# Kernel optimization log

Hardware: AMD Instinct MI355X
Metric: run time of the kernel (lower is better)

Reference implementation:

```python
import math
import jax, jax.numpy as jnp
import numpy as np
from jax import lax

B, S, D = 2, 1024, 768
H, E, DH = 12, 8, 64          # n_head, num_experts, head dim
KA = 1                        # top-k experts per head (attention)
KF = 2                        # top-k experts per token (FFN)
DFF = 2048
EMA_DECAY = 0.99
CAP_FACTOR = 1.25
NEG_INF = -1e9


def setup_inputs() -> dict:
    key = jax.random.key(0)
    ks = jax.random.split(key, 16)
    sc = 0.02
    x = jax.random.normal(ks[0], (B, S, D), jnp.float32)
    causal = jnp.tril(jnp.ones((S, S), jnp.float32))
    mask = jnp.where(causal > 0, 0.0, NEG_INF).astype(jnp.float32)
    return {
        "x": x,
        "mask": mask,
        "W_q": jax.random.normal(ks[1], (D, D), jnp.float32) * sc,
        "W_k": jax.random.normal(ks[2], (D, D), jnp.float32) * sc,
        "W_v": jax.random.normal(ks[3], (H, E, DH, DH), jnp.float32) * sc,
        "W_o": jax.random.normal(ks[4], (H, E, DH, DH), jnp.float32) * sc,
        "W_router": jax.random.normal(ks[5], (D, H * E), jnp.float32) * sc,
        "g1": jnp.ones((D,), jnp.float32),
        "b1": jnp.zeros((D,), jnp.float32),
        "g2": jnp.ones((D,), jnp.float32),
        "b2": jnp.zeros((D,), jnp.float32),
        "gate_ff": jax.random.normal(ks[6], (D, E), jnp.float32) * sc,
        "W1": jax.random.normal(ks[7], (E, D, DFF), jnp.float32) * sc,
        "W2": jax.random.normal(ks[8], (E, DFF, D), jnp.float32) * sc,
    }


def layer_norm(x, g, b, eps=1e-5):
    m = jnp.mean(x, -1, keepdims=True)
    v = jnp.var(x, -1, keepdims=True)
    return (x - m) * lax.rsqrt(v + eps) * g + b


def head_switch_attention(x, mask, W_q, W_k, W_v, W_o, W_router):
    b, s, d = x.shape
    q = (x @ W_q).reshape(b, s, H, DH)
    k = (x @ W_k).reshape(b, s, H, DH)
    scores = jnp.einsum("bshd,bthd->bhst", q, k) / math.sqrt(DH) + mask
    p_attn = jax.nn.softmax(scores, axis=-1)          # (B,H,S,S)
    gate_logits = (x @ W_router).reshape(b, s, H, E)
    topk_scores, topk_idx = lax.top_k(gate_logits, KA)  # (B,S,H,KA)
    probs = jax.nn.softmax(topk_scores, axis=-1)
    x_h = x.reshape(b, s, H, DH)
    # value projections for all experts (small d_h x d_h GEMMs)
    v_all = jnp.einsum("bshd,hedf->bshef", x_h, W_v)
    y = jnp.zeros_like(x_h)
    hard_counts = jnp.zeros((H, E), jnp.float32)
    for slot in range(KA):
        oh = jax.nn.one_hot(topk_idx[..., slot], E, dtype=x.dtype)  # (B,S,H,E)
        v_sel = jnp.einsum("bshef,bshe->bshf", v_all, oh)
        # faithful to original einsum 'bhst,hbsd->hbtd' (sums over s)
        attn_out = jnp.einsum("bhst,bshf->bthf", p_attn, v_sel)
        o_all = jnp.einsum("bthf,hefg->btheg", attn_out, W_o)
        o_sel = jnp.einsum("btheg,bthe->bthg", o_all, oh)
        y = y + o_sel * probs[..., slot][..., None]
        hard_counts = hard_counts + lax.stop_gradient(oh).sum((0, 1))
    y = y.reshape(b, s, d)
    # EMA buffers start at zero -> ema = (1-decay)*hard/denom
    ema = hard_counts / (b * s * KA) * (1.0 - EMA_DECAY)
    p_lb = ema / (ema.sum() + 1e-9)
    aux = (p_lb * p_lb).sum() * E * H
    return y, aux


def moe_ffn(x, gate_ff, W1, W2):
    b, s, d = x.shape
    gate_logits = x @ gate_ff                      # (B,S,E), eval: no noise
    topk_scores, topk_idx = lax.top_k(gate_logits, KF)
    probs = jax.nn.softmax(topk_scores, axis=-1)   # (B,S,KF)
    capacity = math.ceil(CAP_FACTOR * (b * s) / E)
    flat_idx = topk_idx.reshape(-1)                # (B*S*KF,)
    oh_flat = jax.nn.one_hot(flat_idx, E, dtype=jnp.float32)
    tokens_so_far = jnp.cumsum(oh_flat, axis=0)
    keep = jnp.take_along_axis(tokens_so_far <= capacity, flat_idx[:, None], axis=1)[:, 0]
    probs = probs * keep.reshape(b, s, KF).astype(probs.dtype)
    probs = probs / (probs.sum(-1, keepdims=True) + 1e-9)
    oh = jax.nn.one_hot(topk_idx, E, dtype=probs.dtype)   # (B,S,KF,E)
    w = (probs[..., None] * oh).sum(2).reshape(b * s, E)  # combined weight per (token, expert)
    xf = x.reshape(b * s, d)
    yf = jnp.zeros_like(xf)
    for e in range(E):
        # scaling applied BEFORE ReLU, matching original x_sel = x * weight
        xe = xf * w[:, e:e + 1]
        yf = yf + jnp.maximum(xe @ W1[e], 0.0) @ W2[e]
    token_ctr = ((probs > 0)[..., None].astype(jnp.float32) * oh).sum((0, 1, 2))
    imp_ctr = (probs[..., None] * oh).sum((0, 1, 2))
    aux = ((token_ctr / token_ctr.sum()) * (imp_ctr / imp_ctr.sum())).sum() * E
    return yf.reshape(b, s, d), aux


def reference(x, mask, W_q, W_k, W_v, W_o, W_router, g1, b1, g2, b2, gate_ff, W1, W2):
    # pre-norm transformer block: x + Attn(LN(x)); x + MoEFFN(LN(x))
    a, aux1 = head_switch_attention(layer_norm(x, g1, b1), mask, W_q, W_k, W_v, W_o, W_router)
    x1 = x + a  # dropout is identity in eval
    f, aux2 = moe_ffn(layer_norm(x1, g2, b2), gate_ff, W1, W2)
    return x1 + f, aux1 + aux2
```

## Files before the change

kernel.cpp:

```cpp
#include <hip/hip_runtime.h>
#include <hip/hip_bf16.h>
#include <cstdint>

typedef __hip_bfloat16 bf16;
typedef __attribute__((ext_vector_type(8))) __bf16 bfrag;
typedef __attribute__((ext_vector_type(4))) float f32x4;

#define B_    2
#define S_    1024
#define D_    768
#define H_    12
#define E_    8
#define DH_   64
#define DFF_  2048
#define CAP_  320
#define CAPP_ 384
#define NTOK  (B_*S_)
#define NTH   (NTOK*H_)
#define QKLD  1536

__device__ __forceinline__ void stage16(const bf16* g, bf16* ldsLane){
#if __has_builtin(__builtin_amdgcn_global_load_lds)
  __builtin_amdgcn_global_load_lds((const __attribute__((address_space(1))) unsigned int*)g,
                                   (__attribute__((address_space(3))) unsigned int*)ldsLane, 16, 0, 0);
#else
  *(bfrag*)ldsLane = *(const bfrag*)g;
#endif
}

__global__ __launch_bounds__(256)
void transp_cvt(const float* __restrict__ src, bf16* __restrict__ dst,
                int K, int N, long sSrc, long sDst, int dstRowOff)
{
  src += (long)blockIdx.z*sSrc;
  dst += (long)blockIdx.z*sDst;
  __shared__ float t[32][33];
  int n0 = blockIdx.x*32, k0 = blockIdx.y*32;
  int tx = threadIdx.x & 31, ty = threadIdx.x >> 5;
#pragma unroll
  for (int r=0;r<4;r++){
    int kk = k0 + ty + r*8, nn = n0 + tx;
    t[ty+r*8][tx] = (nn < N) ? src[(long)kk*N + nn] : 0.f;
  }
  __syncthreads();
#pragma unroll
  for (int r=0;r<4;r++){
    int nn = n0 + ty + r*8;
    if (nn < N) dst[(long)(dstRowOff + nn)*K + k0 + tx] = __float2bfloat16(t[tx][ty+r*8]);
  }
}

__global__ __launch_bounds__(256)
void transp_f32(const float* __restrict__ src, float* __restrict__ dst, int K, int N)
{
  __shared__ float t[32][33];
  int n0 = blockIdx.x*32, k0 = blockIdx.y*32;
  int tx = threadIdx.x & 31, ty = threadIdx.x >> 5;
#pragma unroll
  for (int r=0;r<4;r++){
    int kk = k0 + ty + r*8, nn = n0 + tx;
    t[ty+r*8][tx] = (nn < N) ? src[(long)kk*N + nn] : 0.f;
  }
  __syncthreads();
#pragma unroll
  for (int r=0;r<4;r++){
    int nn = n0 + ty + r*8;
    if (nn < N) dst[(long)nn*K + k0 + tx] = t[tx][ty+r*8];
  }
}

__global__ __launch_bounds__(256)
void gemm_bn64(const bf16* __restrict__ A, const bf16* __restrict__ Bt, void* __restrict__ C,
               int M, int N, int K, long sA, long sB, long sC, int relu, int outBf)
{
  A  += (long)blockIdx.z*sA;
  Bt += (long)blockIdx.z*sB;
  int m0 = blockIdx.y*128, n0 = blockIdx.x*64;
  __shared__ bf16 As[128*32];
  __shared__ bf16 Bs[64*32];
  int tid = threadIdx.x;
  int w = tid >> 6, lane = tid & 63;
  int quad = lane >> 4, l16 = lane & 15;
  int wm = w*32;
  f32x4 acc[2][4] = {};
  int srow = (lane >> 2);
  int gsw  = ((lane & 3) ^ (srow & 3))*8;
  const bf16* aBase = A + (long)m0*K;
  const bf16* bBase = Bt + (long)n0*K;
  int xr = (l16 & 3);
  for (int k0=0; k0<K; k0+=32){
#pragma unroll
    for (int j=0;j<2;j++){
      int c = w*2 + j;
      int row = c*16 + srow;
      stage16(aBase + (long)row*K + k0 + gsw, As + c*512 + lane*8);
    }
    {
      int row = w*16 + srow;
      stage16(bBase + (long)row*K + k0 + gsw, Bs + w*512 + lane*8);
    }
    __syncthreads();
    bfrag af[2], bfv[4];
#pragma unroll
    for (int t=0;t<2;t++) af[t]  = *(const bfrag*)(As + (wm + t*16 + l16)*32 + ((quad ^ xr)*8));
#pragma unroll
    for (int t=0;t<4;t++) bfv[t] = *(const bfrag*)(Bs + (t*16 + l16)*32 + ((quad ^ xr)*8));
#pragma unroll
    for (int ti=0;ti<2;ti++)
#pragma unroll
      for (int tj=0;tj<4;tj++)
        acc[ti][tj] = __builtin_amdgcn_mfma_f32_16x16x32_bf16(af[ti], bfv[tj], acc[ti][tj], 0, 0, 0);
    __syncthreads();
  }
  long zoff = (long)blockIdx.z*sC;
  if (outBf){
    bf16* Cb = (bf16*)C + zoff;
#pragma unroll
    for (int ti=0;ti<2;ti++)
#pragma unroll
      for (int tj=0;tj<4;tj++)
#pragma unroll
        for (int r=0;r<4;r++){
          int row = m0 + wm + ti*16 + quad*4 + r;
          int col = n0 + tj*16 + l16;
          float v = acc[ti][tj][r];
          if (relu) v = fmaxf(v, 0.f);
          Cb[(long)row*N + col] = __float2bfloat16(v);
        }
  } else {
    float* Cf = (float*)C + zoff;
#pragma unroll
    for (int ti=0;ti<2;ti++)
#pragma unroll
      for (int tj=0;tj<4;tj++)
#pragma unroll
        for (int r=0;r<4;r++){
          int row = m0 + wm + ti*16 + quad*4 + r;
          int col = n0 + tj*16 + l16;
          float v = acc[ti][tj][r];
          if (relu) v = fmaxf(v, 0.f);
          Cf[(long)row*N + col] = v;
        }
  }
}

__global__ __launch_bounds__(256)
void ln_kernel(const float* __restrict__ src, const float* __restrict__ g, const float* __restrict__ bb,
               float* __restrict__ dstF, bf16* __restrict__ dstB,
               const float* __restrict__ gateW, float* __restrict__ glog2)
{
  int row = blockIdx.x, tid = threadIdx.x;
  __shared__ float red[256];
  __shared__ float gsum[4][E_];
  float v[3];
#pragma unroll
  for (int j=0;j<3;j++) v[j] = src[(long)row*D_ + tid + j*256];
  float s = v[0]+v[1]+v[2];
  red[tid]=s; __syncthreads();
  for (int o=128;o>0;o>>=1){ if(tid<o) red[tid]+=red[tid+o]; __syncthreads(); }
  float mean = red[0]*(1.0f/D_);
  __syncthreads();
  float sq = 0.f;
#pragma unroll
  for (int j=0;j<3;j++){ float d=v[j]-mean; sq += d*d; }
  red[tid]=sq; __syncthreads();
  for (int o=128;o>0;o>>=1){ if(tid<o) red[tid]+=red[tid+o]; __syncthreads(); }
  float rstd = rsqrtf(red[0]*(1.0f/D_) + 1e-5f);
  float ov[3];
#pragma unroll
  for (int j=0;j<3;j++){
    int d = tid + j*256;
    float o = (v[j]-mean)*rstd*g[d] + bb[d];
    ov[j] = o;
    dstF[(long)row*D_+d] = o;
    if (dstB) dstB[(long)row*D_+d] = __float2bfloat16(o);
  }
  if (gateW){
    float gp[E_] = {};
#pragma unroll
    for (int j=0;j<3;j++){
      int d = tid + j*256;
      const float* gw = gateW + (long)d*E_;
#pragma unroll
      for (int e=0;e<E_;e++) gp[e] += ov[j]*gw[e];
    }
#pragma unroll
    for (int off=1; off<64; off<<=1)
#pragma unroll
      for (int e=0;e<E_;e++) gp[e] += __shfl_xor(gp[e], off);
    if ((tid & 63) == 0)
#pragma unroll
      for (int e=0;e<E_;e++) gsum[tid>>6][e] = gp[e];
    __syncthreads();
    if (tid < E_)
      glog2[(long)row*E_ + tid] = gsum[0][tid]+gsum[1][tid]+gsum[2][tid]+gsum[3][tid];
  }
}

#define RTOK 4
__global__ __launch_bounds__(768)
void router_argmax(const float* __restrict__ ln1, const float* __restrict__ WrT,
                   int* __restrict__ eidx, int* __restrict__ gHist)
{
  int tok0 = blockIdx.x*RTOK;
  int tid = threadIdx.x;
  int col = tid >> 3, seg = tid & 7;
  __shared__ float xrow[RTOK][D_];
  __shared__ float logits[RTOK][96];
  for (int i=tid; i<RTOK*D_; i+=768){
    int t = i / D_, dpos = i - t*D_;
    xrow[t][dpos] = ln1[(long)(tok0+t)*D_ + dpos];
  }
  __syncthreads();
  const float* wrow = WrT + (long)col*D_;
  float acc[RTOK] = {};
#pragma unroll
  for (int j=0;j<24;j++){
    int dbase = j*32 + seg*4;
    float4 w = *(const float4*)(wrow + dbase);
#pragma unroll
    for (int t=0;t<RTOK;t++){
      float4 xv = *(const float4*)(&xrow[t][dbase]);
      acc[t] += xv.x*w.x + xv.y*w.y + xv.z*w.z + xv.w*w.w;
    }
  }
#pragma unroll
  for (int off=1; off<8; off<<=1)
#pragma unroll
    for (int t=0;t<RTOK;t++) acc[t] += __shfl_xor(acc[t], off);
  if (seg == 0)
#pragma unroll
    for (int t=0;t<RTOK;t++) logits[t][col] = acc[t];
  __syncthreads();
  if (tid < RTOK*H_){
    int t = tid / H_, h = tid % H_;
    const float* p = &logits[t][h*8];
    float best = p[0]; int bi = 0;
#pragma unroll
    for (int e=1;e<8;e++){ float v=p[e]; if (v > best){ best=v; bi=e; } }
    eidx[(tok0+t)*H_ + h] = bi;
    atomicAdd(&gHist[h*E_ + bi], 1);
  }
}

__global__ __launch_bounds__(64)
void vsel_kernel(const float* __restrict__ ln1, const float* __restrict__ Wv,
                 const int* __restrict__ eidx, bf16* __restrict__ vT)
{
  int blk = blockIdx.x;
  int h = blk % H_, tok = blk / H_;
  int b = tok >> 10, s = tok & 1023;
  int f = threadIdx.x;
  __shared__ float xs[DH_];
  xs[f] = ln1[(long)tok*D_ + h*DH_ + f];
  __syncthreads();
  int e = eidx[blk];
  const float* W = Wv + (long)(h*E_+e)*DH_*DH_;
  float acc = 0.f;
#pragma unroll 8
  for (int d=0; d<DH_; d++) acc += xs[d]*W[d*DH_ + f];
  vT[((long)(b*H_+h)*DH_ + f)*S_ + s] = __float2bfloat16(acc);
}

__global__ __launch_bounds__(256)
void attn_stats_mfma(const bf16* __restrict__ qkB, float* __restrict__ gM, float* __restrict__ gL)
{
  int s0 = blockIdx.x*64;
  int h = blockIdx.y, b = blockIdx.z;
  int tid = threadIdx.x;
  int w = tid >> 6, lane = tid & 63;
  int quad = lane >> 4, l16 = lane & 15;
  int x7 = l16 & 7;
  __shared__ bf16 ldsQ[64*64];
  __shared__ bf16 ldsK[64*64];
  const bf16* qbase = qkB + ((long)(b*S_ + s0))*QKLD + h*DH_;
#pragma unroll
  for (int j=0;j<2;j++){
    int c = j*256 + tid;
    int row = c >> 3;
    int gs = ((c & 7) ^ (row & 7))*8;
    stage16(qbase + (long)row*QKLD + gs, ldsQ + c*8);
  }
  float m_run[4] = {-1e30f,-1e30f,-1e30f,-1e30f};
  float l_run[4] = {0.f,0.f,0.f,0.f};
  const bf16* kbase = qkB + ((long)(b*S_))*QKLD + 768 + h*DH_;
  int ttEnd = s0 >> 6;
  for (int tt=0; tt<=ttEnd; tt++){
    __syncthreads();
#pragma unroll
    for (int j=0;j<2;j++){
      int c = j*256 + tid;
      int row = c >> 3;
      int gs = ((c & 7) ^ (row & 7))*8;
      stage16(kbase + (long)(tt*64 + row)*QKLD + gs, ldsK + c*8);
    }
    __syncthreads();
    bfrag af0 = *(const bfrag*)(ldsQ + (w*16 + l16)*64 + ((quad     ^ x7)*8));
    bfrag af1 = *(const bfrag*)(ldsQ + (w*16 + l16)*64 + (((quad+4) ^ x7)*8));
    f32x4 cfr[4];
#pragma unroll
    for (int j=0;j<4;j++){
      bfrag b0 = *(const bfrag*)(ldsK + (j*16 + l16)*64 + ((quad     ^ x7)*8));
      bfrag b1 = *(const bfrag*)(ldsK + (j*16 + l16)*64 + (((quad+4) ^ x7)*8));
      f32x4 z = {};
      z = __builtin_amdgcn_mfma_f32_16x16x32_bf16(af0, b0, z, 0,0,0);
      z = __builtin_amdgcn_mfma_f32_16x16x32_bf16(af1, b1, z, 0,0,0);
      cfr[j] = z;
    }
#pragma unroll
    for (int r=0;r<4;r++){
      int s_g = s0 + w*16 + quad*4 + r;
      float v[4];
#pragma unroll
      for (int j=0;j<4;j++){
        int t_g = tt*64 + j*16 + l16;
        v[j] = (t_g <= s_g) ? cfr[j][r]*0.125f : -1e30f;
      }
      float mt = fmaxf(fmaxf(v[0],v[1]), fmaxf(v[2],v[3]));
#pragma unroll
      for (int mm=1; mm<16; mm<<=1) mt = fmaxf(mt, __shfl_xor(mt, mm));
      float mn = fmaxf(m_run[r], mt);
      float sum = __expf(v[0]-mn)+__expf(v[1]-mn)+__expf(v[2]-mn)+__expf(v[3]-mn);
#pragma unroll
      for (int mm=1; mm<16; mm<<=1) sum += __shfl_xor(sum, mm);
      l_run[r] = l_run[r]*__expf(m_run[r]-mn) + sum;
      m_run[r] = mn;
    }
  }
  if (l16 == 0){
    long base = ((long)(b*H_ + h))*S_ + s0 + w*16 + quad*4;
#pragma unroll
    for (int r=0;r<4;r++){ gM[base+r] = m_run[r]; gL[base+r] = l_run[r]; }
  }
}

__global__ __launch_bounds__(256)
void attn_pv(const bf16* __restrict__ qkB, const bf16* __restrict__ vT,
             const float* __restrict__ gM, const float* __restrict__ gL, float* __restrict__ aoH)
{
  int t0 = blockIdx.x*64;
  int h = blockIdx.y, b = blockIdx.z;
  int bh = b*H_ + h;
  int tid = threadIdx.x;
  int w = tid >> 6, lane = tid & 63;
  int quad = lane >> 4, l16 = lane & 15;
  int x7 = l16 & 7;
  __shared__ bf16 ldsK[64*64];
  __shared__ bf16 ldsQ[64*64];
  __shared__ bf16 ldsV[64*64];
  __shared__ bf16 ldsS[64*72];
  __shared__ float smx[64], sli[64];
  const bf16* kbase = qkB + ((long)(b*S_ + t0))*QKLD + 768 + h*DH_;
#pragma unroll
  for (int j=0;j<2;j++){
    int c = j*256 + tid;
    int row = c >> 3;
    int gs = ((c & 7) ^ (row & 7))*8;
    stage16(kbase + (long)row*QKLD + gs, ldsK + c*8);
  }
  f32x4 accO[4] = {};
  const bf16* qbase = qkB + ((long)(b*S_))*QKLD + h*DH_;
  const bf16* vbase = vT + ((long)bh*DH_)*S_;
  for (int sb = t0>>6; sb < S_/64; sb++){
    __syncthreads();
#pragma unroll
    for (int j=0;j<2;j++){
      int c = j*256 + tid;
      int row = c >> 3;
      int gs = ((c & 7) ^ (row & 7))*8;
      stage16(qbase + (long)(sb*64 + row)*QKLD + gs, ldsQ + c*8);
      stage16(vbase + (long)row*S_ + sb*64 + gs, ldsV + c*8);
    }
    if (tid < 64){
      smx[tid] = gM[(long)bh*S_ + sb*64 + tid];
      sli[tid] = 1.0f / gL[(long)bh*S_ + sb*64 + tid];
    }
    __syncthreads();
    bfrag af0 = *(const bfrag*)(ldsK + (w*16 + l16)*64 + ((quad     ^ x7)*8));
    bfrag af1 = *(const bfrag*)(ldsK + (w*16 + l16)*64 + (((quad+4) ^ x7)*8));
    f32x4 cs[4];
#pragma unroll
    for (int j=0;j<4;j++){
      bfrag b0 = *(const bfrag*)(ldsQ + (j*16 + l16)*64 + ((quad     ^ x7)*8));
      bfrag b1 = *(const bfrag*)(ldsQ + (j*16 + l16)*64 + (((quad+4) ^ x7)*8));
      f32x4 z = {};
      z = __builtin_amdgcn_mfma_f32_16x16x32_bf16(af0, b0, z, 0,0,0);
      z = __builtin_amdgcn_mfma_f32_16x16x32_bf16(af1, b1, z, 0,0,0);
      cs[j] = z;
    }
#pragma unroll
    for (int j=0;j<4;j++)
#pragma unroll
      for (int r=0;r<4;r++){
        int t_loc = w*16 + quad*4 + r;
        int s_loc = j*16 + l16;
        float wgt = ((t0 + t_loc) <= (sb*64 + s_loc))
                  ? __expf(cs[j][r]*0.125f - smx[s_loc])*sli[s_loc] : 0.f;
        ldsS[t_loc*72 + s_loc] = __float2bfloat16(wgt);
      }
    bfrag pa0 = *(const bfrag*)(ldsS + (w*16 + l16)*72 + quad*8);
    bfrag pa1 = *(const bfrag*)(ldsS + (w*16 + l16)*72 + 32 + quad*8);
#pragma unroll
    for (int j=0;j<4;j++){
      bfrag b0 = *(const bfrag*)(ldsV + (j*16 + l16)*64 + ((quad     ^ x7)*8));
      bfrag b1 = *(const bfrag*)(ldsV + (j*16 + l16)*64 + (((quad+4) ^ x7)*8));
      accO[j] = __builtin_amdgcn_mfma_f32_16x16x32_bf16(pa0, b0, accO[j], 0,0,0);
      accO[j] = __builtin_amdgcn_mfma_f32_16x16x32_bf16(pa1, b1, accO[j], 0,0,0);
    }
  }
#pragma unroll
  for (int j=0;j<4;j++)
#pragma unroll
    for (int r=0;r<4;r++){
      int t_loc = w*16 + quad*4 + r;
      int f = j*16 + l16;
      aoH[((long)bh*S_ + t0 + t_loc)*DH_ + f] = accO[j][r];
    }
}

__global__ __launch_bounds__(64)
void oproj_kernel(const float* __restrict__ aoH, const float* __restrict__ Wo,
                  const int* __restrict__ eidx, const float* __restrict__ x,
                  float* __restrict__ x1)
{
  int blk = blockIdx.x;
  int h = blk % H_, tok = blk / H_;
  int b = tok >> 10, s = tok & 1023;
  int g = threadIdx.x;
  __shared__ float xs[DH_];
  xs[g] = aoH[((long)(b*H_+h)*S_ + s)*DH_ + g];
  __syncthreads();
  int e = eidx[blk];
  const float* W = Wo + (long)(h*E_+e)*DH_*DH_;
  float acc = 0.f;
#pragma unroll 8
  for (int f=0; f<DH_; f++) acc += xs[f]*W[f*DH_ + g];
  long idx = (long)tok*D_ + h*DH_ + g;
  x1[idx] = x[idx] + acc;
}

__global__ __launch_bounds__(256)
void route_kernel(const float* __restrict__ glog2, const int* __restrict__ gHist,
                  int* __restrict__ gI0, int* __restrict__ gI1,
                  int* __restrict__ gPos0, int* __restrict__ gPos1,
                  int* __restrict__ listTok, float* __restrict__ listW,
                  int* __restrict__ gCnt, float* __restrict__ auxOut)
{
  __shared__ unsigned char sI0[NTOK], sI1[NTOK];
  __shared__ float sP0[NTOK], sP1[NTOK];
  __shared__ short sPos0[NTOK], sPos1[NTOK];
  __shared__ int   sScan[256*E_];
  __shared__ int   sHist[H_*E_];
  __shared__ float sImp[E_];
  __shared__ int   sCnt[E_];
  int tid = threadIdx.x;
  if (tid < E_) sImp[tid] = 0.f;
  if (tid < H_*E_) sHist[tid] = gHist[tid];
  for (int i=tid; i<NTOK; i+=256){
    const float* p = glog2 + (long)i*E_;
    float b0 = p[0]; int e0 = 0;
#pragma unroll
    for (int e=1;e<E_;e++){ float vv=p[e]; if (vv > b0){ b0=vv; e0=e; } }
    float b1v = -1e30f; int e1 = 0;
#pragma unroll
    for (int e=0;e<E_;e++){ if (e==e0) continue; float vv=p[e]; if (vv > b1v){ b1v=vv; e1=e; } }
    float ex = __expf(b1v - b0);
    float inv = 1.f/(1.f + ex);
    sI0[i] = (unsigned char)e0; sI1[i] = (unsigned char)e1;
    sP0[i] = inv; sP1[i] = ex*inv;
    gI0[i] = e0; gI1[i] = e1;
  }
  __syncthreads();
  {
    int myCnt[E_] = {};
#pragma unroll
    for (int j=0;j<16;j++){
      int i = tid*16 + j;
      int tok = i >> 1;
      int e = (i & 1) ? (int)sI1[tok] : (int)sI0[tok];
      myCnt[e]++;
    }
#pragma unroll
    for (int e=0;e<E_;e++) sScan[tid*E_+e] = myCnt[e];
    __syncthreads();
    for (int off=1; off<256; off<<=1){
      int v[E_];
      if (tid >= off){
#pragma unroll
        for (int e=0;e<E_;e++) v[e] = sScan[(tid-off)*E_+e];
      }
      __syncthreads();
      if (tid >= off){
#pragma unroll
        for (int e=0;e<E_;e++) sScan[tid*E_+e] += v[e];
      }
      __syncthreads();
    }
    int pref[E_];
#pragma unroll
    for (int e=0;e<E_;e++) pref[e] = tid ? sScan[(tid-1)*E_+e] : 0;
#pragma unroll
    for (int j=0;j<16;j++){
      int i = tid*16 + j;
      int tok = i >> 1;
      int e = (i & 1) ? (int)sI1[tok] : (int)sI0[tok];
      int pos = pref[e]++;
      short p = (pos < CAP_) ? (short)pos : (short)-1;
      if (i & 1) sPos1[tok] = p; else sPos0[tok] = p;
    }
    if (tid < E_){
      int cnt = sScan[255*E_ + tid];
      sCnt[tid] = cnt < CAP_ ? cnt : CAP_;
      gCnt[tid] = sCnt[tid];
    }
  }
  __syncthreads();
  for (int i=tid; i<NTOK; i+=256){
    int e0 = sI0[i], e1 = sI1[i];
    int p0i = sPos0[i], p1i = sPos1[i];
    float k0 = p0i >= 0 ? 1.f : 0.f, k1 = p1i >= 0 ? 1.f : 0.f;
    float p0 = sP0[i], p1 = sP1[i];
    float denom = p0*k0 + p1*k1 + 1e-9f;
    float w0 = p0*k0/denom, w1 = p1*k1/denom;
    if (p0i >= 0){ listTok[e0*CAP_+p0i] = i; listW[e0*CAP_+p0i] = w0; atomicAdd(&sImp[e0], w0); }
    if (p1i >= 0){ listTok[e1*CAP_+p1i] = i; listW[e1*CAP_+p1i] = w1; atomicAdd(&sImp[e1], w1); }
    gPos0[i] = p0i; gPos1[i] = p1i;
  }
  __syncthreads();
  if (tid == 0){
    float tot = 0.f;
    for (int i=0;i<H_*E_;i++) tot += (float)sHist[i]*(1.0f/NTOK)*0.01f;
    float a1 = 0.f;
    for (int i=0;i<H_*E_;i++){
      float p = ((float)sHist[i]*(1.0f/NTOK)*0.01f)/(tot + 1e-9f);
      a1 += p*p;
    }
    a1 *= (float)(H_*E_);
    float tcs = 0.f, ims = 0.f;
    for (int e=0;e<E_;e++){ tcs += (float)sCnt[e]; ims += sImp[e]; }
    float a2 = 0.f;
    for (int e=0;e<E_;e++) a2 += ((float)sCnt[e]/tcs)*(sImp[e]/ims);
    a2 *= (float)E_;
    auxOut[0] = a1 + a2;
  }
}

__global__ __launch_bounds__(256)
void gather_kernel(const float* __restrict__ ln2, const int* __restrict__ listTok,
                   const float* __restrict__ listW, const int* __restrict__ gCnt,
                   bf16* __restrict__ Xg)
{
  int blk = blockIdx.x;
  int e = blk / CAPP_, r = blk % CAPP_;
  int tid = threadIdx.x;
  bool live = r < gCnt[e];
  int tok = 0; float w = 0.f;
  if (live){ tok = listTok[e*CAP_+r]; w = listW[e*CAP_+r]; }
  for (int d=tid; d<D_; d+=256)
    Xg[(long)blk*D_ + d] = __float2bfloat16(live ? ln2[(long)tok*D_+d]*w : 0.f);
}

__global__ __launch_bounds__(256)
void combine_kernel(const float* __restrict__ x1, const float* __restrict__ Yexp,
                    const int* __restrict__ gI0, const int* __restrict__ gI1,
                    const int* __restrict__ gPos0, const int* __restrict__ gPos1,
                    float* __restrict__ out)
{
  int i = blockIdx.x;
  int tid = threadIdx.x;
  int p0 = gPos0[i], p1 = gPos1[i];
  int e0 = gI0[i],  e1 = gI1[i];
  const float* y0 = Yexp + (long)(e0*CAPP_ + (p0 >= 0 ? p0 : 0))*D_;
  const float* y1 = Yexp + (long)(e1*CAPP_ + (p1 >= 0 ? p1 : 0))*D_;
  for (int d=tid; d<D_; d+=256){
    float v = x1[(long)i*D_+d];
    if (p0 >= 0) v += y0[d];
    if (p1 >= 0) v += y1[d];
    out[(long)i*D_+d] = v;
  }
}

extern "C" void kernel_launch(void* const* d_in, const int* in_sizes, int n_in,
                              void* d_out, int out_size, void* d_ws, size_t ws_size,
                              hipStream_t stream)
{
  const float* x    = (const float*)d_in[0];
  const float* W_q  = (const float*)d_in[2];
  const float* W_k  = (const float*)d_in[3];
  const float* W_v  = (const float*)d_in[4];
  const float* W_o  = (const float*)d_in[5];
  const float* W_r  = (const float*)d_in[6];
  const float* g1   = (const float*)d_in[7];
  const float* b1   = (const float*)d_in[8];
  const float* g2   = (const float*)d_in[9];
  const float* b2   = (const float*)d_in[10];
  const float* gate = (const float*)d_in[11];
  const float* W1   = (const float*)d_in[12];
  const float* W2   = (const float*)d_in[13];
  float* out = (float*)d_out;

  float* wsf = (float*)d_ws;
  const long oX1   = 0;
  const long oLnF  = 1572864;
  const long oLnB  = 3145728;
  const long oWcat = 3932160;
  const long oWrT  = 4521984;
  const long oHist = 4595712;
  const long oGM   = 4718592;
  const long oGL   = 4743168;
  const long oEidx = 4767744;
  const long oGlg2 = 4792320;
  const long oI0   = 4808704;
  const long oI1   = 4810752;
  const long oP0   = 4812800;
  const long oP1   = 4814848;
  const long oLT   = 4816896;
  const long oLW   = 4819456;
  const long oCnt  = 4822016;
  const long SB    = 4822528;
  const long TOTAL = SB + 12976128;
  if (ws_size < (size_t)TOTAL*4) return;

  float* x1    = wsf + oX1;
  float* lnbF  = wsf + oLnF;
  bf16*  lnbB  = (bf16*)(wsf + oLnB);
  bf16*  WcatB = (bf16*)(wsf + oWcat);
  float* WrT   = wsf + oWrT;
  int*   gHist = (int*)(wsf + oHist);
  float* gM    = wsf + oGM;
  float* gL    = wsf + oGL;
  int*   eidx  = (int*)(wsf + oEidx);
  float* glog2 = wsf + oGlg2;
  int*   gI0   = (int*)(wsf + oI0);
  int*   gI1   = (int*)(wsf + oI1);
  int*   gPos0 = (int*)(wsf + oP0);
  int*   gPos1 = (int*)(wsf + oP1);
  int*   lTok  = (int*)(wsf + oLT);
  float* lW    = wsf + oLW;
  int*   gCnt  = (int*)(wsf + oCnt);
  bf16*  qkB   = (bf16*)(wsf + SB);
  bf16*  vT    = (bf16*)(wsf + SB + 1572864);
  float* aoH   = wsf + SB + 2359296;
  bf16*  WT    = (bf16*)(wsf + SB);
  bf16*  Xg    = (bf16*)(wsf + SB + 6291456);
  bf16*  Hid   = (bf16*)(wsf + SB + 7471104);
  float* Yexp  = wsf + SB + 10616832;

  hipMemsetAsync(gHist, 0, H_*E_*sizeof(int), stream);
  transp_cvt<<<dim3(24,24,1),256,0,stream>>>(W_q, WcatB, 768, 768, 0, 0, 0);
  transp_cvt<<<dim3(24,24,1),256,0,stream>>>(W_k, WcatB, 768, 768, 0, 0, 768);
  transp_f32<<<dim3(3,24,1),256,0,stream>>>(W_r, WrT, 768, 96);

  ln_kernel<<<NTOK,256,0,stream>>>(x, g1, b1, lnbF, lnbB, nullptr, nullptr);
  gemm_bn64<<<dim3(24,16,1),256,0,stream>>>(lnbB, WcatB, qkB, 2048, QKLD, 768, 0,0,0, 0, 1);
  router_argmax<<<NTOK/RTOK,768,0,stream>>>(lnbF, WrT, eidx, gHist);
  vsel_kernel<<<NTH,64,0,stream>>>(lnbF, W_v, eidx, vT);
  attn_stats_mfma<<<dim3(S_/64,H_,B_),256,0,stream>>>(qkB, gM, gL);
  attn_pv<<<dim3(S_/64,H_,B_),256,0,stream>>>(qkB, vT, gM, gL, aoH);
  oproj_kernel<<<NTH,64,0,stream>>>(aoH, W_o, eidx, x, x1);

  ln_kernel<<<NTOK,256,0,stream>>>(x1, g2, b2, lnbF, nullptr, gate, glog2);
  route_kernel<<<1,256,0,stream>>>(glog2, gHist, gI0,gI1,gPos0,gPos1, lTok,lW,gCnt, out + (size_t)NTOK*D_);
  gather_kernel<<<E_*CAPP_,256,0,stream>>>(lnbF, lTok, lW, gCnt, Xg);
  transp_cvt<<<dim3(64,24,8),256,0,stream>>>(W1, WT, 768, 2048, (long)768*2048, (long)2048*768, 0);
  gemm_bn64<<<dim3(32,3,8),256,0,stream>>>(Xg, WT, Hid, CAPP_, DFF_, 768,
                                           (long)CAPP_*768, (long)2048*768, (long)CAPP_*2048, 1, 1);
  transp_cvt<<<dim3(24,64,8),256,0,stream>>>(W2, WT, 2048, 768, (long)2048*768, (long)768*2048, 0);
  gemm_bn64<<<dim3(12,3,8),256,0,stream>>>(Hid, WT, Yexp, CAPP_, 768, 2048,
                                           (long)CAPP_*2048, (long)768*2048, (long)CAPP_*768, 0, 0);
  combine_kernel<<<NTOK,256,0,stream>>>(x1, Yexp, gI0,gI1,gPos0,gPos1, out);
}
```

Baseline: 439.2 us.

## Split-K the FFN down-projection GEMM and remap workgroups across XCDs

Measured after the change: 421.2 us. -4.1%, faster.

```diff
diff --git a/kernel.cpp b/kernel.cpp
--- a/kernel.cpp
+++ b/kernel.cpp
@@ -70,12 +70,22 @@
 }
 
 __global__ __launch_bounds__(256)
-void gemm_bn64(const bf16* __restrict__ A, const bf16* __restrict__ Bt, void* __restrict__ C,
-               int M, int N, int K, long sA, long sB, long sC, int relu, int outBf)
-{
-  A  += (long)blockIdx.z*sA;
-  Bt += (long)blockIdx.z*sB;
-  int m0 = blockIdx.y*128, n0 = blockIdx.x*64;
+void gemm_bn64(const bf16* __restrict__ A, const bf16* __restrict__ Bt,
+               void* __restrict__ C, void* __restrict__ C2,
+               int M, int N, int K, long sA, long sB, long sC, int relu, int outBf, int kSplit)
+{
+  int nwg = gridDim.x*gridDim.y*gridDim.z;
+  int bid = blockIdx.x + gridDim.x*(blockIdx.y + gridDim.y*blockIdx.z);
+  int nid = (bid & 7)*(nwg >> 3) + (bid >> 3);
+  int bx = nid % gridDim.x;
+  int t1 = nid / gridDim.x;
+  int by = t1 % gridDim.y;
+  int bz = t1 / gridDim.y;
+  int e  = bz / kSplit, kc = bz - e*kSplit;
+  A  += (long)e*sA;
+  Bt += (long)e*sB;
+  int kLen = K / kSplit, kBase = kc*kLen;
+  int m0 = by*128, n0 = bx*64;
   __shared__ bf16 As[128*32];
   __shared__ bf16 Bs[64*32];
   int tid = threadIdx.x;
@@ -88,7 +98,7 @@
   const bf16* aBase = A + (long)m0*K;
   const bf16* bBase = Bt + (long)n0*K;
   int xr = (l16 & 3);
-  for (int k0=0; k0<K; k0+=32){
+  for (int k0=kBase; k0<kBase+kLen; k0+=32){
 #pragma unroll
     for (int j=0;j<2;j++){
       int c = w*2 + j;
@@ -112,9 +122,10 @@
         acc[ti][tj] = __builtin_amdgcn_mfma_f32_16x16x32_bf16(af[ti], bfv[tj], acc[ti][tj], 0, 0, 0);
     __syncthreads();
   }
-  long zoff = (long)blockIdx.z*sC;
+  long zoff = (long)e*sC;
+  void* Cp = kc ? C2 : C;
   if (outBf){
-    bf16* Cb = (bf16*)C + zoff;
+    bf16* Cb = (bf16*)Cp + zoff;
 #pragma unroll
     for (int ti=0;ti<2;ti++)
 #pragma unroll
@@ -128,7 +139,7 @@
           Cb[(long)row*N + col] = __float2bfloat16(v);
         }
   } else {
-    float* Cf = (float*)C + zoff;
+    float* Cf = (float*)Cp + zoff;
 #pragma unroll
     for (int ti=0;ti<2;ti++)
 #pragma unroll
@@ -561,7 +572,8 @@
 }
 
 __global__ __launch_bounds__(256)
-void combine_kernel(const float* __restrict__ x1, const float* __restrict__ Yexp,
+void combine_kernel(const float* __restrict__ x1,
+                    const float* __restrict__ Ya, const float* __restrict__ Yb,
                     const int* __restrict__ gI0, const int* __restrict__ gI1,
                     const int* __restrict__ gPos0, const int* __restrict__ gPos1,
                     float* __restrict__ out)
@@ -570,12 +582,14 @@
   int tid = threadIdx.x;
   int p0 = gPos0[i], p1 = gPos1[i];
   int e0 = gI0[i],  e1 = gI1[i];
-  const float* y0 = Yexp + (long)(e0*CAPP_ + (p0 >= 0 ? p0 : 0))*D_;
-  const float* y1 = Yexp + (long)(e1*CAPP_ + (p1 >= 0 ? p1 : 0))*D_;
+  long off0 = (long)(e0*CAPP_ + (p0 >= 0 ? p0 : 0))*D_;
+  long off1 = (long)(e1*CAPP_ + (p1 >= 0 ? p1 : 0))*D_;
+  const float* y0a = Ya + off0; const float* y0b = Yb + off0;
+  const float* y1a = Ya + off1; const float* y1b = Yb + off1;
   for (int d=tid; d<D_; d+=256){
     float v = x1[(long)i*D_+d];
-    if (p0 >= 0) v += y0[d];
-    if (p1 >= 0) v += y1[d];
+    if (p0 >= 0) v += y0a[d] + y0b[d];
+    if (p1 >= 0) v += y1a[d] + y1b[d];
     out[(long)i*D_+d] = v;
   }
 }
@@ -645,6 +659,7 @@
   bf16*  Xg    = (bf16*)(wsf + SB + 6291456);
   bf16*  Hid   = (bf16*)(wsf + SB + 7471104);
   float* Yexp  = wsf + SB + 10616832;
+  float* YexpB = wsf + oLnF;
 
   hipMemsetAsync(gHist, 0, H_*E_*sizeof(int), stream);
   transp_cvt<<<dim3(24,24,1),256,0,stream>>>(W_q, WcatB, 768, 768, 0, 0, 0);
@@ -652,7 +667,7 @@
   transp_f32<<<dim3(3,24,1),256,0,stream>>>(W_r, WrT, 768, 96);
 
   ln_kernel<<<NTOK,256,0,stream>>>(x, g1, b1, lnbF, lnbB, nullptr, nullptr);
-  gemm_bn64<<<dim3(24,16,1),256,0,stream>>>(lnbB, WcatB, qkB, 2048, QKLD, 768, 0,0,0, 0, 1);
+  gemm_bn64<<<dim3(24,16,1),256,0,stream>>>(lnbB, WcatB, qkB, nullptr, 2048, QKLD, 768, 0,0,0, 0, 1, 1);
   router_argmax<<<NTOK/RTOK,768,0,stream>>>(lnbF, WrT, eidx, gHist);
   vsel_kernel<<<NTH,64,0,stream>>>(lnbF, W_v, eidx, vT);
   attn_stats_mfma<<<dim3(S_/64,H_,B_),256,0,stream>>>(qkB, gM, gL);
@@ -663,10 +678,10 @@
   route_kernel<<<1,256,0,stream>>>(glog2, gHist, gI0,gI1,gPos0,gPos1, lTok,lW,gCnt, out + (size_t)NTOK*D_);
   gather_kernel<<<E_*CAPP_,256,0,stream>>>(lnbF, lTok, lW, gCnt, Xg);
   transp_cvt<<<dim3(64,24,8),256,0,stream>>>(W1, WT, 768, 2048, (long)768*2048, (long)2048*768, 0);
-  gemm_bn64<<<dim3(32,3,8),256,0,stream>>>(Xg, WT, Hid, CAPP_, DFF_, 768,
-                                           (long)CAPP_*768, (long)2048*768, (long)CAPP_*2048, 1, 1);
+  gemm_bn64<<<dim3(32,3,8),256,0,stream>>>(Xg, WT, Hid, nullptr, CAPP_, DFF_, 768,
+                                           (long)CAPP_*768, (long)2048*768, (long)CAPP_*2048, 1, 1, 1);
   transp_cvt<<<dim3(24,64,8),256,0,stream>>>(W2, WT, 2048, 768, (long)2048*768, (long)768*2048, 0);
-  gemm_bn64<<<dim3(12,3,8),256,0,stream>>>(Hid, WT, Yexp, CAPP_, 768, 2048,
-                                           (long)CAPP_*2048, (long)768*2048, (long)CAPP_*768, 0, 0);
-  combine_kernel<<<NTOK,256,0,stream>>>(x1, Yexp, gI0,gI1,gPos0,gPos1, out);
-}
+  gemm_bn64<<<dim3(12,3,16),256,0,stream>>>(Hid, WT, Yexp, YexpB, CAPP_, 768, 2048,
+                                            (long)CAPP_*2048, (long)768*2048, (long)CAPP_*768, 0, 0, 2);
+  combine_kernel<<<NTOK,256,0,stream>>>(x1, Yexp, YexpB, gI0,gI1,gPos0,gPos1, out);
+}
```
